# Kernel tuning notes

Hardware: AMD Instinct MI355X
Metric: run time of the kernel (lower is better)

Reference implementation:

```python
import jax, jax.numpy as jnp
import numpy as np

B, S, D, H = 32, 2048, 512, 512

def setup_inputs() -> dict:
    key = jax.random.key(0)
    kx, kq, kk, kv = jax.random.split(key, 4)
    scale = 1.0 / np.sqrt(D)
    x = jax.random.normal(kx, (B, S, D), dtype=jnp.float32)
    Wq = jax.random.normal(kq, (D, H), dtype=jnp.float32) * scale
    Wk = jax.random.normal(kk, (D, H), dtype=jnp.float32) * scale
    Wv = jax.random.normal(kv, (D, H), dtype=jnp.float32) * scale
    return {"x": x, "Wq": Wq, "Wk": Wk, "Wv": Wv}

def reference(x, Wq, Wk, Wv):
    # Linear projections (bias=False)
    q = jnp.einsum('bsd,dh->bsh', x, Wq)
    k = jnp.einsum('bsd,dh->bsh', x, Wk)
    v = jnp.einsum('bsd,dh->bsh', x, Wv)
    # Pairwise KL(p_i || q_j) with p = softmax(q_i), q = softmax(k_j):
    #   KL = sum_h p_i log p_i  -  sum_h p_i log q_j
    # The first term is a per-row negative entropy; the second is a GEMM,
    # avoiding the original O(S^2) Python double loop.
    logp = jax.nn.log_softmax(q, axis=-1)          # [B,S,H]
    p = jnp.exp(logp)
    logq = jax.nn.log_softmax(k, axis=-1)          # [B,S,H]
    neg_ent = jnp.sum(p * logp, axis=-1)           # [B,S]
    cross = jnp.einsum('bih,bjh->bij', p, logq)    # [B,S,S]
    kl_divs = neg_ent[:, :, None] - cross          # [B,S,S]
    attn_weights = jax.nn.softmax(-kl_divs, axis=-1)
    attn_output = jnp.einsum('bij,bjh->bih', attn_weights, v)
    return attn_output
```

## Files before the change

kernel.cpp:

```cpp
#include <hip/hip_runtime.h>
#include <hip/hip_bf16.h>

typedef __bf16 bf16x8 __attribute__((ext_vector_type(8)));
typedef float  f32x4  __attribute__((ext_vector_type(4)));

#define NB 32
#define NS 2048
#define ND 512
#define NH 512
#define NROWS (NB*NS)
#define L2E 1.44269504f

__device__ __forceinline__ void gload16(const void* g, void* l) {
  __builtin_amdgcn_global_load_lds((const __attribute__((address_space(1))) void*)g,
                                   (__attribute__((address_space(3))) void*)l, 16, 0, 0);
}

__global__ void prep_w(const float* __restrict__ Wq, const float* __restrict__ Wk,
                       const float* __restrict__ Wv, __bf16* __restrict__ wT) {
  int i = blockIdx.x * blockDim.x + threadIdx.x;
  const int total = 3 * ND * NH;
  for (; i < total; i += gridDim.x * blockDim.x) {
    int m = i / (ND * NH);
    int rem = i - m * (ND * NH);
    int h = rem >> 9;
    int d = rem & 511;
    const float* W = (m == 0) ? Wq : ((m == 1) ? Wk : Wv);
    wT[i] = (__bf16)W[(size_t)d * NH + h];
  }
}

#define K1_XOFF 0
#define K1_WOFF 65536
#define K1_REDM 131072
#define K1_REDS 132096
#define K1_LDS  133120

__global__ __launch_bounds__(512, 2)
void proj_kernel(const float* __restrict__ x, const __bf16* __restrict__ wT,
                 __bf16* __restrict__ p_out, __bf16* __restrict__ k_out,
                 float* __restrict__ L_out, __bf16* __restrict__ vt_out)
{
  __shared__ __align__(16) char smem[K1_LDS];
  char* xb = smem + K1_XOFF;
  char* wb = smem + K1_WOFF;
  float* redm = (float*)(smem + K1_REDM);
  float* reds = (float*)(smem + K1_REDS);

  const int tid = threadIdx.x;
  const int lane = tid & 63, l15 = lane & 15, g = lane >> 4;
  const int w = tid >> 6, rt = w & 1, cs = w >> 1;
  const int r0 = blockIdx.x * 64;
  const int b = r0 >> 11, s0 = r0 & (NS - 1);

  {
    int row = tid >> 3, sc = tid & 7;
    const float* xr = x + (size_t)(r0 + row) * ND;
    #pragma unroll
    for (int u = 0; u < 8; ++u) {
      int s = u * 8 + sc;
      float4 v0 = *(const float4*)(xr + s * 8);
      float4 v1 = *(const float4*)(xr + s * 8 + 4);
      bf16x8 cv;
      cv[0]=(__bf16)v0.x; cv[1]=(__bf16)v0.y; cv[2]=(__bf16)v0.z; cv[3]=(__bf16)v0.w;
      cv[4]=(__bf16)v1.x; cv[5]=(__bf16)v1.y; cv[6]=(__bf16)v1.z; cv[7]=(__bf16)v1.w;
      *(bf16x8*)(xb + row * 1024 + ((s ^ (row & 7)) * 16)) = cv;
    }
  }
  {
    #pragma unroll
    for (int u = 0; u < 4; ++u) {
      int sid = u * 512 + tid, h = sid >> 2, gg = sid & 3;
      gload16(wT + (size_t)h * ND + ((gg ^ ((h >> 1) & 3)) * 8), wb + sid * 16);
    }
  }
  __syncthreads();

  for (int m = 0; m < 3; ++m) {
    f32x4 acc[2][8];
    #pragma unroll
    for (int i2 = 0; i2 < 2; ++i2)
      #pragma unroll
      for (int ht = 0; ht < 8; ++ht) acc[i2][ht] = (f32x4){0.f,0.f,0.f,0.f};

    for (int step = 0; step < 16; ++step) {
      int gs = m * 16 + step;
      char* wcur = wb + (gs & 1) * 32768;
      if (gs + 1 < 48) {
        int gn = gs + 1, mn = gn >> 4, sn = gn & 15;
        const __bf16* wsrc = wT + (size_t)mn * (ND * NH) + sn * 32;
        char* wdst = wb + (gn & 1) * 32768;
        #pragma unroll
        for (int u = 0; u < 4; ++u) {
          int sid = u * 512 + tid, h = sid >> 2, gg = sid & 3;
          gload16(wsrc + (size_t)h * ND + ((gg ^ ((h >> 1) & 3)) * 8), wdst + sid * 16);
        }
      }
      bf16x8 a0, a1;
      {
        int ar = rt * 32 + l15;
        a0 = *(const bf16x8*)(xb + ar * 1024 + (((step * 4 + g) ^ (ar & 7)) * 16));
        ar += 16;
        a1 = *(const bf16x8*)(xb + ar * 1024 + (((step * 4 + g) ^ (ar & 7)) * 16));
      }
      #pragma unroll
      for (int ht = 0; ht < 8; ++ht) {
        int h = cs * 128 + ht * 16 + l15;
        bf16x8 bb = *(const bf16x8*)(wcur + h * 64 + ((g ^ ((h >> 1) & 3)) * 16));
        acc[0][ht] = __builtin_amdgcn_mfma_f32_16x16x32_bf16(a0, bb, acc[0][ht], 0, 0, 0);
        acc[1][ht] = __builtin_amdgcn_mfma_f32_16x16x32_bf16(a1, bb, acc[1][ht], 0, 0, 0);
      }
      __syncthreads();
    }

    if (m == 2) {
      #pragma unroll
      for (int i2 = 0; i2 < 2; ++i2) {
        int sgg = (s0 >> 3) + rt * 4 + i2 * 2 + (g >> 1);
        size_t basep = ((size_t)(b * 256 + sgg)) * 512;
        #pragma unroll
        for (int ht = 0; ht < 8; ++ht) {
          int h = cs * 128 + ht * 16 + l15;
          union { __bf16 h4[4]; ushort4 u4; } cv;
          #pragma unroll
          for (int r = 0; r < 4; ++r) cv.h4[r] = (__bf16)acc[i2][ht][r];
          *(ushort4*)(vt_out + (basep + h) * 8 + (g & 1) * 4) = cv.u4;
        }
      }
    } else {
      float mrow[2][4], tsum[2][4];
      #pragma unroll
      for (int i2 = 0; i2 < 2; ++i2)
        #pragma unroll
        for (int r = 0; r < 4; ++r) {
          float v = acc[i2][0][r];
          #pragma unroll
          for (int ht = 1; ht < 8; ++ht) v = fmaxf(v, acc[i2][ht][r]);
          v = fmaxf(v, __shfl_xor(v, 1)); v = fmaxf(v, __shfl_xor(v, 2));
          v = fmaxf(v, __shfl_xor(v, 4)); v = fmaxf(v, __shfl_xor(v, 8));
          if (l15 == 0) redm[cs * 64 + rt * 32 + i2 * 16 + g * 4 + r] = v;
        }
      __syncthreads();
      #pragma unroll
      for (int i2 = 0; i2 < 2; ++i2)
        #pragma unroll
        for (int r = 0; r < 4; ++r) {
          int row = rt * 32 + i2 * 16 + g * 4 + r;
          mrow[i2][r] = fmaxf(fmaxf(redm[row], redm[64 + row]),
                              fmaxf(redm[128 + row], redm[192 + row]));
        }
      #pragma unroll
      for (int i2 = 0; i2 < 2; ++i2)
        #pragma unroll
        for (int r = 0; r < 4; ++r) {
          float s = 0.f;
          #pragma unroll
          for (int ht = 0; ht < 8; ++ht) s += exp2f((acc[i2][ht][r] - mrow[i2][r]) * L2E);
          s += __shfl_xor(s, 1); s += __shfl_xor(s, 2);
          s += __shfl_xor(s, 4); s += __shfl_xor(s, 8);
          if (l15 == 0) reds[cs * 64 + rt * 32 + i2 * 16 + g * 4 + r] = s;
        }
      __syncthreads();
      #pragma unroll
      for (int i2 = 0; i2 < 2; ++i2)
        #pragma unroll
        for (int r = 0; r < 4; ++r) {
          int row = rt * 32 + i2 * 16 + g * 4 + r;
          tsum[i2][r] = reds[row] + reds[64 + row] + reds[128 + row] + reds[192 + row];
        }
      __bf16* dst = (m == 0) ? p_out : k_out;
      if (m == 0) {
        #pragma unroll
        for (int i2 = 0; i2 < 2; ++i2) {
          float inv[4];
          #pragma unroll
          for (int r = 0; r < 4; ++r) inv[r] = 1.f / tsum[i2][r];
          #pragma unroll
          for (int ht = 0; ht < 8; ++ht) {
            int col = cs * 128 + ht * 16 + l15;
            #pragma unroll
            for (int r = 0; r < 4; ++r) {
              int row = rt * 32 + i2 * 16 + g * 4 + r;
              dst[(size_t)(r0 + row) * NH + col] =
                  (__bf16)(exp2f((acc[i2][ht][r] - mrow[i2][r]) * L2E) * inv[r]);
            }
          }
        }
      } else {
        #pragma unroll
        for (int i2 = 0; i2 < 2; ++i2)
          #pragma unroll
          for (int ht = 0; ht < 8; ++ht) {
            int col = cs * 128 + ht * 16 + l15;
            #pragma unroll
            for (int r = 0; r < 4; ++r) {
              int row = rt * 32 + i2 * 16 + g * 4 + r;
              dst[(size_t)(r0 + row) * NH + col] = (__bf16)acc[i2][ht][r];
            }
          }
        if (cs == 0 && l15 == 0) {
          #pragma unroll
          for (int i2 = 0; i2 < 2; ++i2)
            #pragma unroll
            for (int r = 0; r < 4; ++r) {
              int row = rt * 32 + i2 * 16 + g * 4 + r;
              L_out[r0 + row] = mrow[i2][r] + __logf(tsum[i2][r]);
            }
        }
      }
      __syncthreads();
    }
  }
}

#define QOFF 0
#define KOFF 65536
#define PSTR 512
#define A_LDS 163840

__global__ __launch_bounds__(512, 2)
void attn_kernel(const __bf16* __restrict__ p_all, const __bf16* __restrict__ k_all,
                 const float* __restrict__ L_all, const __bf16* __restrict__ vt_all,
                 float* __restrict__ out)
{
  __shared__ __align__(16) char smem[A_LDS];
  char* Qb = smem + QOFF;
  float* lred = (float*)(smem + KOFF);

  const int bid = blockIdx.x;
  const int b = ((bid >> 8) << 3) + (bid & 7);
  const int ib = (bid >> 3) & 31;
  const int i0 = ib * 64;

  const __bf16* Pg = p_all + (size_t)b * NS * NH;
  const __bf16* Kg = k_all + (size_t)b * NS * NH;
  const float*  Lg = L_all + (size_t)b * NS;
  const __bf16* Vg = vt_all + (size_t)b * (256 * 512 * 8);
  float* Og = out + ((size_t)b * NS + i0) * NH;

  const int tid = threadIdx.x;
  const int lane = tid & 63, l15 = lane & 15, g = lane >> 4;
  const int w = tid >> 6;
  const int ig = w >> 2, jg = w & 3;
  const int hs = w * 64;
  const int xr = l15 & 7;

  #define STAGE(SS) { \
    int j0_ = ((SS) >> 3) * 256, kh_ = (SS) & 7; \
    char* kd_ = smem + KOFF + ((SS) % 3) * 32768; \
    _Pragma("unroll") \
    for (int u_ = 0; u_ < 4; ++u_) { \
      int sid_ = u_ * 512 + tid, jj_ = sid_ >> 3, s8_ = sid_ & 7; \
      gload16(Kg + (size_t)(j0_ + jj_) * NH + kh_ * 64 + ((s8_ ^ (jj_ & 7)) * 8), \
              kd_ + sid_ * 16); \
    } }

  #pragma unroll
  for (int u = 0; u < 8; ++u) {
    int sid = u * 512 + tid, row = sid >> 6, s = sid & 63;
    int sp = (s & 56) | ((s ^ row) & 7);
    gload16(Pg + (size_t)(i0 + row) * NH + sp * 8, Qb + sid * 16);
  }
  STAGE(0);
  STAGE(1);

  f32x4 o_[4][4];
  #pragma unroll
  for (int it = 0; it < 4; ++it)
    #pragma unroll
    for (int ht = 0; ht < 4; ++ht) o_[it][ht] = (f32x4){0.f,0.f,0.f,0.f};
  float lsum[2][4] = {{0.f,0.f,0.f,0.f},{0.f,0.f,0.f,0.f}};

  #define LOADV(DST, JKS) { \
    _Pragma("unroll") \
    for (int ht_ = 0; ht_ < 4; ++ht_) { \
      int h_ = hs + ht_ * 16 + l15; \
      int sg_ = outer * 32 + (JKS) * 4 + g; \
      (DST)[ht_] = *(const bf16x8*)(Vg + ((size_t)sg_ * 512 + h_) * 8); \
    } }
  #define PVSTEP(JKS, VF) { \
    __builtin_amdgcn_s_setprio(1); \
    _Pragma("unroll") \
    for (int it_ = 0; it_ < 4; ++it_) { \
      int row_ = it_ * 16 + l15; \
      int sp_ = ((JKS) * 4 + g) ^ xr; \
      bf16x8 pa_ = *(const bf16x8*)(Pb + row_ * PSTR + sp_ * 16); \
      _Pragma("unroll") \
      for (int ht_ = 0; ht_ < 4; ++ht_) \
        o_[it_][ht_] = __builtin_amdgcn_mfma_f32_16x16x32_bf16(pa_, (VF)[ht_], o_[it_][ht_], 0, 0, 0); \
    } \
    __builtin_amdgcn_s_setprio(0); }

  for (int outer = 0; outer < 8; ++outer) {
    const int j0 = outer * 256;
    f32x4 acc[2][4];
    #pragma unroll
    for (int i2 = 0; i2 < 2; ++i2)
      #pragma unroll
      for (int jt = 0; jt < 4; ++jt) acc[i2][jt] = (f32x4){0.f,0.f,0.f,0.f};

    #pragma unroll
    for (int kk = 0; kk < 8; ++kk) {
      const int ss = outer * 8 + kk;
      asm volatile("s_waitcnt vmcnt(4)" ::: "memory");
      __builtin_amdgcn_sched_barrier(0);
      __builtin_amdgcn_s_barrier();
      __builtin_amdgcn_sched_barrier(0);
      if (ss + 2 < 64) STAGE(ss + 2);
      const char* rb = smem + KOFF + (ss % 3) * 32768;
      #pragma unroll
      for (int sub = 0; sub < 2; ++sub) {
        bf16x8 a0, a1, bq[4];
        {
          int row0 = ig * 32 + l15;
          int seg = kk * 8 + sub * 4 + g;
          a0 = *(const bf16x8*)(Qb + row0 * 1024 + ((seg ^ (row0 & 7)) * 16));
          a1 = *(const bf16x8*)(Qb + (row0 + 16) * 1024 + ((seg ^ ((row0 + 16) & 7)) * 16));
        }
        #pragma unroll
        for (int jt = 0; jt < 4; ++jt) {
          int j = jg * 64 + jt * 16 + l15;
          bq[jt] = *(const bf16x8*)(rb + j * 128 + (((sub * 4 + g) ^ xr) * 16));
        }
        __builtin_amdgcn_s_setprio(1);
        #pragma unroll
        for (int jt = 0; jt < 4; ++jt) {
          acc[0][jt] = __builtin_amdgcn_mfma_f32_16x16x32_bf16(a0, bq[jt], acc[0][jt], 0, 0, 0);
          acc[1][jt] = __builtin_amdgcn_mfma_f32_16x16x32_bf16(a1, bq[jt], acc[1][jt], 0, 0, 0);
        }
        __builtin_amdgcn_s_setprio(0);
      }
    }

    __builtin_amdgcn_sched_barrier(0);
    __builtin_amdgcn_s_barrier();
    __builtin_amdgcn_sched_barrier(0);
    char* Pb = smem + KOFF + ((outer * 8 + 7) % 3) * 32768;

    {
      float LB[4];
      #pragma unroll
      for (int jt = 0; jt < 4; ++jt) LB[jt] = Lg[j0 + jg * 64 + jt * 16 + l15] * L2E;
      #pragma unroll
      for (int i2 = 0; i2 < 2; ++i2)
        #pragma unroll
        for (int jt = 0; jt < 4; ++jt)
          #pragma unroll
          for (int r = 0; r < 4; ++r) {
            float pv = exp2f(acc[i2][jt][r] * L2E - LB[jt]);
            lsum[i2][r] += pv;
            float other = __shfl_xor(pv, 1);
            if ((l15 & 1) == 0) {
              union { __bf16 h; unsigned short u; } lo, hi;
              lo.h = (__bf16)pv; hi.h = (__bf16)other;
              unsigned int pk = (unsigned int)lo.u | ((unsigned int)hi.u << 16);
              int row = ig * 32 + i2 * 16 + g * 4 + r;
              int d = jg * 32 + jt * 8 + (l15 >> 1);
              int s2 = (d >> 2) ^ (row & 7);
              *(unsigned int*)(Pb + row * PSTR + s2 * 16 + (d & 3) * 4) = pk;
            }
          }
    }
    bf16x8 vA[4], vB[4];
    LOADV(vA, 0); LOADV(vB, 1);
    asm volatile("s_waitcnt lgkmcnt(0)" ::: "memory");
    __builtin_amdgcn_sched_barrier(0);
    __builtin_amdgcn_s_barrier();
    __builtin_amdgcn_sched_barrier(0);

    PVSTEP(0, vA); LOADV(vA, 2);
    PVSTEP(1, vB); LOADV(vB, 3);
    PVSTEP(2, vA); LOADV(vA, 4);
    PVSTEP(3, vB); LOADV(vB, 5);
    PVSTEP(4, vA); LOADV(vA, 6);
    PVSTEP(5, vB); LOADV(vB, 7);
    PVSTEP(6, vA);
    PVSTEP(7, vB);
  }

  __syncthreads();
  #pragma unroll
  for (int i2 = 0; i2 < 2; ++i2)
    #pragma unroll
    for (int r = 0; r < 4; ++r) {
      float v = lsum[i2][r];
      v += __shfl_xor(v, 1); v += __shfl_xor(v, 2);
      v += __shfl_xor(v, 4); v += __shfl_xor(v, 8);
      if (l15 == 0) lred[jg * 64 + ig * 32 + i2 * 16 + g * 4 + r] = v;
    }
  __syncthreads();

  #pragma unroll
  for (int it = 0; it < 4; ++it) {
    float inv[4];
    #pragma unroll
    for (int r = 0; r < 4; ++r) {
      int row = it * 16 + g * 4 + r;
      inv[r] = 1.f / (lred[row] + lred[64 + row] + lred[128 + row] + lred[192 + row]);
    }
    #pragma unroll
    for (int ht = 0; ht < 4; ++ht)
      #pragma unroll
      for (int r = 0; r < 4; ++r) {
        int row = it * 16 + g * 4 + r;
        Og[(size_t)row * NH + hs + ht * 16 + l15] = o_[it][ht][r] * inv[r];
      }
  }
}

extern "C" void kernel_launch(void* const* d_in, const int* in_sizes, int n_in,
                              void* d_out, int out_size, void* d_ws, size_t ws_size,
                              hipStream_t stream) {
  const float* x  = (const float*)d_in[0];
  const float* Wq = (const float*)d_in[1];
  const float* Wk = (const float*)d_in[2];
  const float* Wv = (const float*)d_in[3];
  float* out = (float*)d_out;
  char* ws = (char*)d_ws;

  size_t off = 0;
  __bf16* wT   = (__bf16*)(ws + off); off += (size_t)3 * ND * NH * 2;
  __bf16* p_ws = (__bf16*)(ws + off); off += (size_t)NROWS * NH * 2;
  __bf16* k_ws = (__bf16*)(ws + off); off += (size_t)NROWS * NH * 2;
  __bf16* vt_ws= (__bf16*)(ws + off); off += (size_t)NROWS * NH * 2;
  float*  L_ws = (float*)(ws + off);  off += (size_t)NROWS * 4;

  prep_w<<<dim3(512), dim3(256), 0, stream>>>(Wq, Wk, Wv, wT);
  proj_kernel<<<dim3(1024), dim3(512), 0, stream>>>(x, wT, p_ws, k_ws, L_ws, vt_ws);
  attn_kernel<<<dim3(1024), dim3(512), 0, stream>>>(p_ws, k_ws, L_ws, vt_ws, out);
}
```

Baseline: 660.4 us.

## Triple-buffer weight loads in projection and restage attention K prefetch across PV phase

The projection kernel moves from a double-buffered weight pipeline with a full __syncthreads per step to a three-slot ring with two stages in flight. It waits on vmcnt and a raw s_barrier, and raises MFMA priority. Reduction scratch now reuses the weight buffer region, and LDS grows to 160KB with launch bounds dropped to one block per CU. In the attention kernel, K-tile prefetch no longer crosses the outer-loop boundary; the next outer iteration's first two K stages are issued during the PV phase instead. This should overlap loads with compute, at the cost of halved occupancy in both kernels.

```diff
diff --git a/kernel.cpp b/kernel.cpp
--- a/kernel.cpp
+++ b/kernel.cpp
@@ -32,11 +32,9 @@
 
 #define K1_XOFF 0
 #define K1_WOFF 65536
-#define K1_REDM 131072
-#define K1_REDS 132096
-#define K1_LDS  133120
-
-__global__ __launch_bounds__(512, 2)
+#define K1_LDS  163840
+
+__global__ __launch_bounds__(512, 1)
 void proj_kernel(const float* __restrict__ x, const __bf16* __restrict__ wT,
                  __bf16* __restrict__ p_out, __bf16* __restrict__ k_out,
                  float* __restrict__ L_out, __bf16* __restrict__ vt_out)
@@ -44,8 +42,6 @@
   __shared__ __align__(16) char smem[K1_LDS];
   char* xb = smem + K1_XOFF;
   char* wb = smem + K1_WOFF;
-  float* redm = (float*)(smem + K1_REDM);
-  float* reds = (float*)(smem + K1_REDS);
 
   const int tid = threadIdx.x;
   const int lane = tid & 63, l15 = lane & 15, g = lane >> 4;
@@ -67,14 +63,17 @@
       *(bf16x8*)(xb + row * 1024 + ((s ^ (row & 7)) * 16)) = cv;
     }
   }
-  {
-    #pragma unroll
-    for (int u = 0; u < 4; ++u) {
-      int sid = u * 512 + tid, h = sid >> 2, gg = sid & 3;
-      gload16(wT + (size_t)h * ND + ((gg ^ ((h >> 1) & 3)) * 8), wb + sid * 16);
-    }
-  }
-  __syncthreads();
+  #define STAGEW(GS) { \
+    int mn_ = (GS) >> 4, sn_ = (GS) & 15; \
+    const __bf16* ws_ = wT + (size_t)mn_ * (ND * NH) + sn_ * 32; \
+    char* wd_ = wb + ((GS) % 3) * 32768; \
+    _Pragma("unroll") \
+    for (int u_ = 0; u_ < 4; ++u_) { \
+      int sid_ = u_ * 512 + tid, h_ = sid_ >> 2, gg_ = sid_ & 3; \
+      gload16(ws_ + (size_t)h_ * ND + ((gg_ ^ ((h_ >> 1) & 3)) * 8), wd_ + sid_ * 16); \
+    } }
+  STAGEW(0);
+  STAGEW(1);
 
   for (int m = 0; m < 3; ++m) {
     f32x4 acc[2][8];
@@ -85,17 +84,14 @@
 
     for (int step = 0; step < 16; ++step) {
       int gs = m * 16 + step;
-      char* wcur = wb + (gs & 1) * 32768;
-      if (gs + 1 < 48) {
-        int gn = gs + 1, mn = gn >> 4, sn = gn & 15;
-        const __bf16* wsrc = wT + (size_t)mn * (ND * NH) + sn * 32;
-        char* wdst = wb + (gn & 1) * 32768;
-        #pragma unroll
-        for (int u = 0; u < 4; ++u) {
-          int sid = u * 512 + tid, h = sid >> 2, gg = sid & 3;
-          gload16(wsrc + (size_t)h * ND + ((gg ^ ((h >> 1) & 3)) * 8), wdst + sid * 16);
-        }
-      }
+      if (gs < 47) { asm volatile("s_waitcnt vmcnt(4) lgkmcnt(0)" ::: "memory"); }
+      else         { asm volatile("s_waitcnt vmcnt(0) lgkmcnt(0)" ::: "memory"); }
+      __builtin_amdgcn_sched_barrier(0);
+      __builtin_amdgcn_s_barrier();
+      __builtin_amdgcn_sched_barrier(0);
+      if (gs + 2 < 48) STAGEW(gs + 2);
+
+      const char* wcur = wb + (gs % 3) * 32768;
       bf16x8 a0, a1;
       {
         int ar = rt * 32 + l15;
@@ -107,10 +103,11 @@
       for (int ht = 0; ht < 8; ++ht) {
         int h = cs * 128 + ht * 16 + l15;
         bf16x8 bb = *(const bf16x8*)(wcur + h * 64 + ((g ^ ((h >> 1) & 3)) * 16));
+        __builtin_amdgcn_s_setprio(1);
         acc[0][ht] = __builtin_amdgcn_mfma_f32_16x16x32_bf16(a0, bb, acc[0][ht], 0, 0, 0);
         acc[1][ht] = __builtin_amdgcn_mfma_f32_16x16x32_bf16(a1, bb, acc[1][ht], 0, 0, 0);
-      }
-      __syncthreads();
+        __builtin_amdgcn_s_setprio(0);
+      }
     }
 
     if (m == 2) {
@@ -128,6 +125,13 @@
         }
       }
     } else {
+      float* redm = (float*)(wb + m * 32768);
+      float* reds = redm + 256;
+      asm volatile("s_waitcnt lgkmcnt(0)" ::: "memory");
+      __builtin_amdgcn_sched_barrier(0);
+      __builtin_amdgcn_s_barrier();
+      __builtin_amdgcn_sched_barrier(0);
+
       float mrow[2][4], tsum[2][4];
       #pragma unroll
       for (int i2 = 0; i2 < 2; ++i2)
@@ -140,7 +144,8 @@
           v = fmaxf(v, __shfl_xor(v, 4)); v = fmaxf(v, __shfl_xor(v, 8));
           if (l15 == 0) redm[cs * 64 + rt * 32 + i2 * 16 + g * 4 + r] = v;
         }
-      __syncthreads();
+      asm volatile("s_waitcnt lgkmcnt(0)" ::: "memory");
+      __builtin_amdgcn_s_barrier();
       #pragma unroll
       for (int i2 = 0; i2 < 2; ++i2)
         #pragma unroll
@@ -160,7 +165,8 @@
           s += __shfl_xor(s, 4); s += __shfl_xor(s, 8);
           if (l15 == 0) reds[cs * 64 + rt * 32 + i2 * 16 + g * 4 + r] = s;
         }
-      __syncthreads();
+      asm volatile("s_waitcnt lgkmcnt(0)" ::: "memory");
+      __builtin_amdgcn_s_barrier();
       #pragma unroll
       for (int i2 = 0; i2 < 2; ++i2)
         #pragma unroll
@@ -208,7 +214,8 @@
             }
         }
       }
-      __syncthreads();
+      asm volatile("s_waitcnt lgkmcnt(0)" ::: "memory");
+      __builtin_amdgcn_s_barrier();
     }
   }
 }
@@ -218,7 +225,7 @@
 #define PSTR 512
 #define A_LDS 163840
 
-__global__ __launch_bounds__(512, 2)
+__global__ __launch_bounds__(512, 1)
 void attn_kernel(const __bf16* __restrict__ p_all, const __bf16* __restrict__ k_all,
                  const float* __restrict__ L_all, const __bf16* __restrict__ vt_all,
                  float* __restrict__ out)
@@ -271,20 +278,18 @@
     for (int ht = 0; ht < 4; ++ht) o_[it][ht] = (f32x4){0.f,0.f,0.f,0.f};
   float lsum[2][4] = {{0.f,0.f,0.f,0.f},{0.f,0.f,0.f,0.f}};
 
-  #define LOADV(DST, JKS) { \
+  #define LOADV(DST, KS) { \
     _Pragma("unroll") \
     for (int ht_ = 0; ht_ < 4; ++ht_) { \
       int h_ = hs + ht_ * 16 + l15; \
-      int sg_ = outer * 32 + (JKS) * 4 + g; \
+      int sg_ = outer * 32 + (KS) * 4 + g; \
       (DST)[ht_] = *(const bf16x8*)(Vg + ((size_t)sg_ * 512 + h_) * 8); \
     } }
-  #define PVSTEP(JKS, VF) { \
+  #define PVSTEP(KS, VF) { \
     __builtin_amdgcn_s_setprio(1); \
     _Pragma("unroll") \
     for (int it_ = 0; it_ < 4; ++it_) { \
-      int row_ = it_ * 16 + l15; \
-      int sp_ = ((JKS) * 4 + g) ^ xr; \
-      bf16x8 pa_ = *(const bf16x8*)(Pb + row_ * PSTR + sp_ * 16); \
+      bf16x8 pa_ = *(const bf16x8*)(Pb + (it_ * 16 + l15) * PSTR + (((KS) * 4 + g) ^ xr) * 16); \
       _Pragma("unroll") \
       for (int ht_ = 0; ht_ < 4; ++ht_) \
         o_[it_][ht_] = __builtin_amdgcn_mfma_f32_16x16x32_bf16(pa_, (VF)[ht_], o_[it_][ht_], 0, 0, 0); \
@@ -302,11 +307,12 @@
     #pragma unroll
     for (int kk = 0; kk < 8; ++kk) {
       const int ss = outer * 8 + kk;
-      asm volatile("s_waitcnt vmcnt(4)" ::: "memory");
-      __builtin_amdgcn_sched_barrier(0);
-      __builtin_amdgcn_s_barrier();
-      __builtin_amdgcn_sched_barrier(0);
-      if (ss + 2 < 64) STAGE(ss + 2);
+      if (kk < 7) { asm volatile("s_waitcnt vmcnt(4)" ::: "memory"); }
+      else        { asm volatile("s_waitcnt vmcnt(0)" ::: "memory"); }
+      __builtin_amdgcn_sched_barrier(0);
+      __builtin_amdgcn_s_barrier();
+      __builtin_amdgcn_sched_barrier(0);
+      if (kk < 6) STAGE(ss + 2);
       const char* rb = smem + KOFF + (ss % 3) * 32768;
       #pragma unroll
       for (int sub = 0; sub < 2; ++sub) {
@@ -374,6 +380,10 @@
     PVSTEP(3, vB); LOADV(vB, 5);
     PVSTEP(4, vA); LOADV(vA, 6);
     PVSTEP(5, vB); LOADV(vB, 7);
+    if (outer < 7) {
+      STAGE(outer * 8 + 8);
+      STAGE(outer * 8 + 9);
+    }
     PVSTEP(6, vA);
     PVSTEP(7, vB);
   }
```

Result: slower. 683.6 us (+3.5%).
